# Performance work log

Measured on AMD Instinct MI355X. Metric: run time of the kernel, lower is better.

The kernel has to match this reference:

```python
import jax, jax.numpy as jnp
import numpy as np

B, N, C, K = 32, 4096, 768, 8

def setup_inputs() -> dict:
    key = jax.random.key(0)
    ks = jax.random.split(key, 5)
    x = jax.random.normal(ks[0], (B, N, C), dtype=jnp.float32)
    ln_gamma = jnp.ones((C,), dtype=jnp.float32)
    ln_beta = jnp.zeros((C,), dtype=jnp.float32)
    W1 = jax.random.normal(ks[1], (C, C), dtype=jnp.float32) / np.sqrt(C)
    b1 = jnp.zeros((C,), dtype=jnp.float32)
    W2 = jax.random.normal(ks[2], (C, K), dtype=jnp.float32) / np.sqrt(C)
    b2 = jnp.zeros((K,), dtype=jnp.float32)
    return {"x": x, "ln_gamma": ln_gamma, "ln_beta": ln_beta,
            "W1": W1, "b1": b1, "W2": W2, "b2": b2}

def reference(x, ln_gamma, ln_beta, W1, b1, W2, b2):
    # LayerNorm over last dim (eps matches torch default 1e-5)
    mu = jnp.mean(x, axis=-1, keepdims=True)
    var = jnp.mean(jnp.square(x - mu), axis=-1, keepdims=True)
    h = (x - mu) * jax.lax.rsqrt(var + 1e-5) * ln_gamma + ln_beta
    # Linear -> exact GELU -> Linear
    h = jax.nn.gelu(h @ W1 + b1, approximate=False)
    logits = h @ W2 + b2  # [B, N, K]
    # softmax over tokens (dim=1)
    attn = jax.nn.softmax(logits, axis=1)
    # weighted token pooling: [B,N,K],[B,N,C] -> [B,K,C]
    return jnp.einsum('bnk,bnc->bkc', attn, x)
```

## Files before the change

### kernel.cpp

```cpp
#include <hip/hip_runtime.h>
#include <hip/hip_fp16.h>

#define M_TOKENS (32*4096)
#define C_DIM 768
#define K_OUT 8

typedef _Float16 f16x8 __attribute__((ext_vector_type(8)));
typedef float f32x4 __attribute__((ext_vector_type(4)));

__device__ __forceinline__ void gl2lds16(const void* g, void* l) {
    __builtin_amdgcn_global_load_lds((const __attribute__((address_space(1))) void*)g,
                                     (__attribute__((address_space(3))) void*)l, 16, 0, 0);
}

__device__ __forceinline__ float gelu_exact(float x) {
    return 0.5f * x * (1.0f + erff(x * 0.70710678118654752440f));
}

__global__ __launch_bounds__(256) void prep_w1(const float* __restrict__ w1,
                                               const float* __restrict__ gamma,
                                               _Float16* __restrict__ w1t) {
    __shared__ float t[64][65];
    const int k0 = blockIdx.x * 64, n0 = blockIdx.y * 64;
    const int c = threadIdx.x & 63, r4 = threadIdx.x >> 6;
#pragma unroll
    for (int p = 0; p < 16; ++p) {
        const int r = p*4 + r4;
        t[r][c] = w1[(size_t)(k0 + r)*C_DIM + n0 + c];
    }
    __syncthreads();
    const float g = gamma[k0 + c];
#pragma unroll
    for (int p = 0; p < 16; ++p) {
        const int n = p*4 + r4;
        w1t[(size_t)(n0 + n)*C_DIM + k0 + c] = (_Float16)(t[c][n] * g);
    }
}

__global__ __launch_bounds__(256) void prep_b1(const float* __restrict__ w1,
                                               const float* __restrict__ beta,
                                               const float* __restrict__ b1,
                                               float* __restrict__ b1p) {
    __shared__ float red[256];
    const int nl = threadIdx.x & 63;
    const int n = blockIdx.x*64 + nl;
    const int part = threadIdx.x >> 6;
    float s = 0.f;
    for (int k = part*192; k < part*192 + 192; ++k)
        s += beta[k] * w1[(size_t)k*C_DIM + n];
    red[threadIdx.x] = s;
    __syncthreads();
    if (part == 0)
        b1p[n] = b1[n] + red[nl] + red[nl+64] + red[nl+128] + red[nl+192];
}


__global__ __launch_bounds__(256) void xnorm_kernel(const float* __restrict__ x,
                                                    _Float16* __restrict__ xn) {
    const int row = blockIdx.x*4 + (threadIdx.x >> 6);
    const int lane = threadIdx.x & 63;
    const float4* xr = (const float4*)(x + (size_t)row * C_DIM);
    float4 v[3];
    float s = 0.f, s2 = 0.f;
#pragma unroll
    for (int i = 0; i < 3; ++i) {
        v[i] = xr[lane + i*64];
        s  += v[i].x + v[i].y + v[i].z + v[i].w;
        s2 += v[i].x*v[i].x + v[i].y*v[i].y + v[i].z*v[i].z + v[i].w*v[i].w;
    }
#pragma unroll
    for (int m = 1; m < 64; m <<= 1) { s += __shfl_xor(s, m); s2 += __shfl_xor(s2, m); }
    const float mu = s * (1.f/768.f);
    const float rs = rsqrtf(s2 * (1.f/768.f) - mu*mu + 1e-5f);
    const float nm = -mu * rs;
    _Float16* xo = xn + (size_t)row * C_DIM;
#pragma unroll
    for (int i = 0; i < 3; ++i) {
        union { _Float16 h[4]; uint2 uu; } pk;
        pk.h[0] = (_Float16)(v[i].x*rs + nm);
        pk.h[1] = (_Float16)(v[i].y*rs + nm);
        pk.h[2] = (_Float16)(v[i].z*rs + nm);
        pk.h[3] = (_Float16)(v[i].w*rs + nm);
        *(uint2*)(xo + (size_t)(lane + i*64)*4) = pk.uu;
    }
}

__global__ __launch_bounds__(256) void gemm1_h_kernel(const _Float16* __restrict__ xn,
        const _Float16* __restrict__ w1t, const float* __restrict__ b1p,
        const float* __restrict__ w2, float* __restrict__ logits) {
    __shared__ __align__(16) union {
        struct { _Float16 a[128*64]; _Float16 b[128*64]; } s;
        _Float16 ht[128*136];
    } u;
    __shared__ float w2s[128*K_OUT];
    __shared__ float b1s[128];

    const int tid = threadIdx.x;
    const int wid = tid >> 6, lane = tid & 63;
    const int l15 = lane & 15, q = lane >> 4;
    const int wm = wid >> 1, wn = wid & 1;
    const int n0 = blockIdx.x * 128;
    const int m0 = blockIdx.y * 128;

    for (int i = tid; i < 128*K_OUT; i += 256) w2s[i] = w2[(size_t)n0*K_OUT + i];
    if (tid < 128) b1s[tid] = b1p[n0 + tid];

    f32x4 acc[4][4] = {};

    for (int kt = 0; kt < 12; ++kt) {
        const int k0 = kt * 64;
#pragma unroll
        for (int i = 0; i < 4; ++i) {
            const int L = i*256 + tid;
            const int row = L >> 3, j = (L & 7) ^ (row & 7);
            gl2lds16(xn + (size_t)(m0 + row)*C_DIM + k0 + j*8,
                     &u.s.a[(i*256 + wid*64)*8]);
        }
#pragma unroll
        for (int i = 0; i < 4; ++i) {
            const int L = i*256 + tid;
            const int row = L >> 3, j = (L & 7) ^ (row & 7);
            gl2lds16(w1t + (size_t)(n0 + row)*C_DIM + k0 + j*8,
                     &u.s.b[(i*256 + wid*64)*8]);
        }
        __syncthreads();
#pragma unroll
        for (int kk = 0; kk < 2; ++kk) {
            f16x8 af[4], bfr[4];
#pragma unroll
            for (int nt = 0; nt < 4; ++nt) {
                const int row = wn*64 + nt*16 + l15;
                const int j = (kk*4 + q) ^ (row & 7);
                af[nt] = *(const f16x8*)&u.s.b[row*64 + j*8];
            }
#pragma unroll
            for (int mt = 0; mt < 4; ++mt) {
                const int row = wm*64 + mt*16 + l15;
                const int j = (kk*4 + q) ^ (row & 7);
                bfr[mt] = *(const f16x8*)&u.s.a[row*64 + j*8];
            }
#pragma unroll
            for (int nt = 0; nt < 4; ++nt)
#pragma unroll
                for (int mt = 0; mt < 4; ++mt)
                    acc[nt][mt] = __builtin_amdgcn_mfma_f32_16x16x32_f16(
                        af[nt], bfr[mt], acc[nt][mt], 0, 0, 0);
        }
        __syncthreads();
    }

#pragma unroll
    for (int nt = 0; nt < 4; ++nt) {
#pragma unroll
        for (int mt = 0; mt < 4; ++mt) {
            const int token = wm*64 + mt*16 + l15;
            const int nl = wn*64 + nt*16 + q*4;
            union { _Float16 h[4]; uint2 uu; } pk;
#pragma unroll
            for (int r = 0; r < 4; ++r)
                pk.h[r] = (_Float16)gelu_exact(acc[nt][mt][r] + b1s[nl + r]);
            *(uint2*)&u.ht[token*136 + nl] = pk.uu;
        }
    }
    __syncthreads();

    f16x8 wf[4];
#pragma unroll
    for (int ks = 0; ks < 4; ++ks) {
        f16x8 t;
#pragma unroll
        for (int j = 0; j < 8; ++j) {
            const int kd = ks*32 + q*8 + j;
            t[j] = (_Float16)((l15 < K_OUT) ? w2s[kd*K_OUT + l15] : 0.f);
        }
        wf[ks] = t;
    }
#pragma unroll
    for (int t2 = 0; t2 < 2; ++t2) {
        const int tt = wid*2 + t2;
        f32x4 p = {};
#pragma unroll
        for (int ks = 0; ks < 4; ++ks) {
            const f16x8 a = *(const f16x8*)&u.ht[(tt*16 + l15)*136 + ks*32 + q*8];
            p = __builtin_amdgcn_mfma_f32_16x16x32_f16(a, wf[ks], p, 0, 0, 0);
        }
        if (l15 < K_OUT) {
#pragma unroll
            for (int r = 0; r < 4; ++r)
                atomicAdd(&logits[(size_t)(m0 + tt*16 + q*4 + r)*K_OUT + l15], p[r]);
        }
    }
}


__global__ __launch_bounds__(256) void stats_kernel(const float* __restrict__ x,
                                                    float2* __restrict__ stats) {
    const int row = blockIdx.x*4 + (threadIdx.x >> 6);
    const int lane = threadIdx.x & 63;
    const float4* xr = (const float4*)(x + (size_t)row * C_DIM);
    float s = 0.f, s2 = 0.f;
#pragma unroll
    for (int i = 0; i < 3; ++i) {
        const float4 v = xr[lane + i*64];
        s  += v.x + v.y + v.z + v.w;
        s2 += v.x*v.x + v.y*v.y + v.z*v.z + v.w*v.w;
    }
#pragma unroll
    for (int m = 1; m < 64; m <<= 1) { s += __shfl_xor(s, m); s2 += __shfl_xor(s2, m); }
    if (lane == 0) {
        const float mu = s * (1.f/768.f);
        const float rs = rsqrtf(s2 * (1.f/768.f) - mu*mu + 1e-5f);
        stats[row] = make_float2(rs, -mu*rs);
    }
}

__global__ __launch_bounds__(256) void gemm1_ln_kernel(const float* __restrict__ x,
        const float2* __restrict__ stats, const _Float16* __restrict__ w1t,
        const float* __restrict__ b1p, const float* __restrict__ w2,
        float* __restrict__ logits) {
    __shared__ __align__(16) union {
        struct { float a[128*64]; _Float16 b[128*64]; } s;
        _Float16 ht[128*136];
    } u;
    __shared__ float w2s[128*K_OUT];
    __shared__ float b1s[128];

    const int tid = threadIdx.x;
    const int wid = tid >> 6, lane = tid & 63;
    const int l15 = lane & 15, q = lane >> 4;
    const int wm = wid >> 1, wn = wid & 1;
    const int n0 = blockIdx.x * 128;
    const int m0 = blockIdx.y * 128;

    for (int i = tid; i < 128*K_OUT; i += 256) w2s[i] = w2[(size_t)n0*K_OUT + i];
    if (tid < 128) b1s[tid] = b1p[n0 + tid];

    float rsL[4], nmL[4];
#pragma unroll
    for (int mt = 0; mt < 4; ++mt) {
        const float2 st = stats[m0 + wm*64 + mt*16 + l15];
        rsL[mt] = st.x; nmL[mt] = st.y;
    }

    f32x4 acc[4][4] = {};

    for (int kt = 0; kt < 12; ++kt) {
        const int k0 = kt * 64;
#pragma unroll
        for (int i = 0; i < 8; ++i) {
            const int L = i*256 + tid;
            const int row = L >> 4, g = (L & 15) ^ (row & 15);
            gl2lds16(x + (size_t)(m0 + row)*C_DIM + k0 + g*4,
                     &u.s.a[(i*256 + wid*64)*4]);
        }
#pragma unroll
        for (int i = 0; i < 4; ++i) {
            const int L = i*256 + tid;
            const int row = L >> 3, j = (L & 7) ^ (row & 7);
            gl2lds16(w1t + (size_t)(n0 + row)*C_DIM + k0 + j*8,
                     &u.s.b[(i*256 + wid*64)*8]);
        }
        __syncthreads();
#pragma unroll
        for (int kk = 0; kk < 2; ++kk) {
            f16x8 af[4], bfr[4];
#pragma unroll
            for (int nt = 0; nt < 4; ++nt) {
                const int row = wn*64 + nt*16 + l15;
                const int j = (kk*4 + q) ^ (row & 7);
                af[nt] = *(const f16x8*)&u.s.b[row*64 + j*8];
            }
#pragma unroll
            for (int mt = 0; mt < 4; ++mt) {
                const int row = wm*64 + mt*16 + l15;
                const int gc = kk*8 + q*2;
                const int c0 = gc ^ (row & 15), c1 = (gc + 1) ^ (row & 15);
                const f32x4 v0 = *(const f32x4*)&u.s.a[row*64 + c0*4];
                const f32x4 v1 = *(const f32x4*)&u.s.a[row*64 + c1*4];
                f16x8 t;
#pragma unroll
                for (int j = 0; j < 4; ++j) {
                    t[j]   = (_Float16)(v0[j]*rsL[mt] + nmL[mt]);
                    t[4+j] = (_Float16)(v1[j]*rsL[mt] + nmL[mt]);
                }
                bfr[mt] = t;
            }
#pragma unroll
            for (int nt = 0; nt < 4; ++nt)
#pragma unroll
                for (int mt = 0; mt < 4; ++mt)
                    acc[nt][mt] = __builtin_amdgcn_mfma_f32_16x16x32_f16(
                        af[nt], bfr[mt], acc[nt][mt], 0, 0, 0);
        }
        __syncthreads();
    }

#pragma unroll
    for (int nt = 0; nt < 4; ++nt) {
#pragma unroll
        for (int mt = 0; mt < 4; ++mt) {
            const int token = wm*64 + mt*16 + l15;
            const int nl = wn*64 + nt*16 + q*4;
            union { _Float16 h[4]; uint2 uu; } pk;
#pragma unroll
            for (int r = 0; r < 4; ++r)
                pk.h[r] = (_Float16)gelu_exact(acc[nt][mt][r] + b1s[nl + r]);
            *(uint2*)&u.ht[token*136 + nl] = pk.uu;
        }
    }
    __syncthreads();

    f16x8 wf[4];
#pragma unroll
    for (int ks = 0; ks < 4; ++ks) {
        f16x8 t;
#pragma unroll
        for (int j = 0; j < 8; ++j) {
            const int kd = ks*32 + q*8 + j;
            t[j] = (_Float16)((l15 < K_OUT) ? w2s[kd*K_OUT + l15] : 0.f);
        }
        wf[ks] = t;
    }
#pragma unroll
    for (int t2 = 0; t2 < 2; ++t2) {
        const int tt = wid*2 + t2;
        f32x4 p = {};
#pragma unroll
        for (int ks = 0; ks < 4; ++ks) {
            const f16x8 a = *(const f16x8*)&u.ht[(tt*16 + l15)*136 + ks*32 + q*8];
            p = __builtin_amdgcn_mfma_f32_16x16x32_f16(a, wf[ks], p, 0, 0, 0);
        }
        if (l15 < K_OUT) {
#pragma unroll
            for (int r = 0; r < 4; ++r)
                atomicAdd(&logits[(size_t)(m0 + tt*16 + q*4 + r)*K_OUT + l15], p[r]);
        }
    }
}

__global__ __launch_bounds__(256) void softmax_kernel(float* p) {
    const int b = blockIdx.x >> 3, k = blockIdx.x & 7;
    const size_t base = ((size_t)b*4096)*K_OUT + k;
    const int tid = threadIdx.x;
    float r[16];
    float mx = -1e30f;
#pragma unroll
    for (int i = 0; i < 16; ++i) {
        r[i] = p[base + (size_t)(tid + i*256)*K_OUT];
        mx = fmaxf(mx, r[i]);
    }
#pragma unroll
    for (int m = 1; m < 64; m <<= 1) mx = fmaxf(mx, __shfl_xor(mx, m));
    __shared__ float redm[4], reds[4];
    if ((tid & 63) == 0) redm[tid >> 6] = mx;
    __syncthreads();
    mx = fmaxf(fmaxf(redm[0], redm[1]), fmaxf(redm[2], redm[3]));
    float s = 0.f;
#pragma unroll
    for (int i = 0; i < 16; ++i) { r[i] = __expf(r[i] - mx); s += r[i]; }
#pragma unroll
    for (int m = 1; m < 64; m <<= 1) s += __shfl_xor(s, m);
    if ((tid & 63) == 0) reds[tid >> 6] = s;
    __syncthreads();
    s = reds[0] + reds[1] + reds[2] + reds[3];
    const float inv = 1.f / s;
#pragma unroll
    for (int i = 0; i < 16; ++i)
        p[base + (size_t)(tid + i*256)*K_OUT] = r[i] * inv;
}

__global__ __launch_bounds__(192) void pool_kernel(const float* __restrict__ x,
        const float* __restrict__ attn, float* __restrict__ out) {
    const int b = blockIdx.x, nc = blockIdx.y;
    const int t0 = nc * 128;
    __shared__ float as_[128*K_OUT];
    for (int i = threadIdx.x; i < 128*K_OUT; i += 192)
        as_[i] = attn[((size_t)b*4096 + t0)*K_OUT + i];
    __syncthreads();
    const int c = threadIdx.x * 4;
    float acc[K_OUT][4] = {};
    const float* xb = x + ((size_t)b*4096 + t0)*C_DIM + c;
    for (int i = 0; i < 128; ++i) {
        const float4 xv = *(const float4*)(xb + (size_t)i*C_DIM);
#pragma unroll
        for (int k = 0; k < K_OUT; ++k) {
            const float a = as_[i*K_OUT + k];
            acc[k][0] += a*xv.x; acc[k][1] += a*xv.y;
            acc[k][2] += a*xv.z; acc[k][3] += a*xv.w;
        }
    }
#pragma unroll
    for (int k = 0; k < K_OUT; ++k)
#pragma unroll
        for (int j = 0; j < 4; ++j)
            atomicAdd(&out[((size_t)b*K_OUT + k)*C_DIM + c + j], acc[k][j]);
}

extern "C" void kernel_launch(void* const* d_in, const int* in_sizes, int n_in,
                              void* d_out, int out_size, void* d_ws, size_t ws_size,
                              hipStream_t stream) {
    const float* x     = (const float*)d_in[0];
    const float* gamma = (const float*)d_in[1];
    const float* beta  = (const float*)d_in[2];
    const float* W1    = (const float*)d_in[3];
    const float* b1    = (const float*)d_in[4];
    const float* W2    = (const float*)d_in[5];
    (void)in_sizes; (void)n_in;

    float* out = (float*)d_out;
    char* ws = (char*)d_ws;

    const size_t XN_BYTES  = (size_t)M_TOKENS * C_DIM * 2;
    const size_t NEED_NEW  = XN_BYTES + 1179648 + 4096 + 4194304;

    if (ws_size >= NEED_NEW) {
        _Float16* xn     = (_Float16*)ws;
        _Float16* w1t    = (_Float16*)(ws + XN_BYTES);
        float*    b1p    = (float*)(ws + XN_BYTES + 1179648);
        float*    logits = (float*)(ws + XN_BYTES + 1179648 + 4096);

        (void)hipMemsetAsync(logits, 0, (size_t)M_TOKENS * K_OUT * 4, stream);
        (void)hipMemsetAsync(d_out, 0, (size_t)out_size * sizeof(float), stream);

        prep_w1<<<dim3(12, 12), 256, 0, stream>>>(W1, gamma, w1t);
        prep_b1<<<12, 256, 0, stream>>>(W1, beta, b1, b1p);
        xnorm_kernel<<<M_TOKENS/4, 256, 0, stream>>>(x, xn);
        gemm1_h_kernel<<<dim3(6, 1024), 256, 0, stream>>>(xn, w1t, b1p, W2, logits);
        softmax_kernel<<<256, 256, 0, stream>>>(logits);
        pool_kernel<<<dim3(32, 32), 192, 0, stream>>>(x, logits, out);
    } else {
        float2*   stats  = (float2*)ws;
        _Float16* w1t    = (_Float16*)(ws + 1048576);
        float*    b1p    = (float*)(ws + 2228224);
        float*    logits = (float*)(ws + 2232320);

        (void)hipMemsetAsync(logits, 0, (size_t)M_TOKENS * K_OUT * 4, stream);
        (void)hipMemsetAsync(d_out, 0, (size_t)out_size * sizeof(float), stream);

        prep_w1<<<dim3(12, 12), 256, 0, stream>>>(W1, gamma, w1t);
        prep_b1<<<12, 256, 0, stream>>>(W1, beta, b1, b1p);
        stats_kernel<<<M_TOKENS/4, 256, 0, stream>>>(x, stats);
        gemm1_ln_kernel<<<dim3(6, 1024), 256, 0, stream>>>(x, stats, w1t, b1p, W2, logits);
        softmax_kernel<<<256, 256, 0, stream>>>(logits);
        pool_kernel<<<dim3(32, 32), 192, 0, stream>>>(x, logits, out);
    }
}
```

Measured before the change: 1.079 ms.

## Use polynomial erf GELU, two rows per xnorm wave, swizzled GEMM tiles, unroll pool

Result: faster. 1.006 ms (-6.8%).

```diff
diff --git a/kernel.cpp b/kernel.cpp
--- a/kernel.cpp
+++ b/kernel.cpp
@@ -13,8 +13,20 @@
                                      (__attribute__((address_space(3))) void*)l, 16, 0, 0);
 }
 
-__device__ __forceinline__ float gelu_exact(float x) {
-    return 0.5f * x * (1.0f + erff(x * 0.70710678118654752440f));
+__device__ __forceinline__ float gelu_fast(float x) {
+    const float z  = x * 0.70710678118654752440f;
+    const float az = fabsf(z);
+    const float t  = __builtin_amdgcn_rcpf(1.0f + 0.3275911f * az);
+    float p = 1.061405429f;
+    p = p * t - 1.453152027f;
+    p = p * t + 1.421413741f;
+    p = p * t - 0.284496736f;
+    p = p * t + 0.254829592f;
+    p = p * t;
+    const float e = __expf(-az * az);
+    const float erf_abs = 1.0f - p * e;
+    const float erf_z = copysignf(erf_abs, z);
+    return 0.5f * x * (1.0f + erf_z);
 }
 
 __global__ __launch_bounds__(256) void prep_w1(const float* __restrict__ w1,
@@ -54,34 +66,49 @@
         b1p[n] = b1[n] + red[nl] + red[nl+64] + red[nl+128] + red[nl+192];
 }
 
-
 __global__ __launch_bounds__(256) void xnorm_kernel(const float* __restrict__ x,
                                                     _Float16* __restrict__ xn) {
-    const int row = blockIdx.x*4 + (threadIdx.x >> 6);
+    const int row0 = blockIdx.x*8 + (threadIdx.x >> 6)*2;
     const int lane = threadIdx.x & 63;
-    const float4* xr = (const float4*)(x + (size_t)row * C_DIM);
-    float4 v[3];
-    float s = 0.f, s2 = 0.f;
+    const float4* xr0 = (const float4*)(x + (size_t)row0 * C_DIM);
+    const float4* xr1 = (const float4*)(x + (size_t)(row0 + 1) * C_DIM);
+    float4 v0[3], v1[3];
+#pragma unroll
+    for (int i = 0; i < 3; ++i) { v0[i] = xr0[lane + i*64]; v1[i] = xr1[lane + i*64]; }
+    float sa = 0.f, s2a = 0.f, sb = 0.f, s2b = 0.f;
 #pragma unroll
     for (int i = 0; i < 3; ++i) {
-        v[i] = xr[lane + i*64];
-        s  += v[i].x + v[i].y + v[i].z + v[i].w;
-        s2 += v[i].x*v[i].x + v[i].y*v[i].y + v[i].z*v[i].z + v[i].w*v[i].w;
-    }
-#pragma unroll
-    for (int m = 1; m < 64; m <<= 1) { s += __shfl_xor(s, m); s2 += __shfl_xor(s2, m); }
-    const float mu = s * (1.f/768.f);
-    const float rs = rsqrtf(s2 * (1.f/768.f) - mu*mu + 1e-5f);
-    const float nm = -mu * rs;
-    _Float16* xo = xn + (size_t)row * C_DIM;
+        sa  += v0[i].x + v0[i].y + v0[i].z + v0[i].w;
+        s2a += v0[i].x*v0[i].x + v0[i].y*v0[i].y + v0[i].z*v0[i].z + v0[i].w*v0[i].w;
+        sb  += v1[i].x + v1[i].y + v1[i].z + v1[i].w;
+        s2b += v1[i].x*v1[i].x + v1[i].y*v1[i].y + v1[i].z*v1[i].z + v1[i].w*v1[i].w;
+    }
+#pragma unroll
+    for (int m = 1; m < 64; m <<= 1) {
+        sa += __shfl_xor(sa, m); s2a += __shfl_xor(s2a, m);
+        sb += __shfl_xor(sb, m); s2b += __shfl_xor(s2b, m);
+    }
+    const float mua = sa * (1.f/768.f);
+    const float rsa = rsqrtf(s2a * (1.f/768.f) - mua*mua + 1e-5f);
+    const float nma = -mua * rsa;
+    const float mub = sb * (1.f/768.f);
+    const float rsb = rsqrtf(s2b * (1.f/768.f) - mub*mub + 1e-5f);
+    const float nmb = -mub * rsb;
+    _Float16* xo0 = xn + (size_t)row0 * C_DIM;
+    _Float16* xo1 = xn + (size_t)(row0 + 1) * C_DIM;
 #pragma unroll
     for (int i = 0; i < 3; ++i) {
         union { _Float16 h[4]; uint2 uu; } pk;
-        pk.h[0] = (_Float16)(v[i].x*rs + nm);
-        pk.h[1] = (_Float16)(v[i].y*rs + nm);
-        pk.h[2] = (_Float16)(v[i].z*rs + nm);
-        pk.h[3] = (_Float16)(v[i].w*rs + nm);
-        *(uint2*)(xo + (size_t)(lane + i*64)*4) = pk.uu;
+        pk.h[0] = (_Float16)(v0[i].x*rsa + nma);
+        pk.h[1] = (_Float16)(v0[i].y*rsa + nma);
+        pk.h[2] = (_Float16)(v0[i].z*rsa + nma);
+        pk.h[3] = (_Float16)(v0[i].w*rsa + nma);
+        *(uint2*)(xo0 + (size_t)(lane + i*64)*4) = pk.uu;
+        pk.h[0] = (_Float16)(v1[i].x*rsb + nmb);
+        pk.h[1] = (_Float16)(v1[i].y*rsb + nmb);
+        pk.h[2] = (_Float16)(v1[i].z*rsb + nmb);
+        pk.h[3] = (_Float16)(v1[i].w*rsb + nmb);
+        *(uint2*)(xo1 + (size_t)(lane + i*64)*4) = pk.uu;
     }
 }
 
@@ -99,8 +126,11 @@
     const int wid = tid >> 6, lane = tid & 63;
     const int l15 = lane & 15, q = lane >> 4;
     const int wm = wid >> 1, wn = wid & 1;
-    const int n0 = blockIdx.x * 128;
-    const int m0 = blockIdx.y * 128;
+
+    const int L = blockIdx.y * 6 + blockIdx.x;
+    const int swz = (L & 7) * 768 + (L >> 3);
+    const int n0 = (swz % 6) * 128;
+    const int m0 = (swz / 6) * 128;
 
     for (int i = tid; i < 128*K_OUT; i += 256) w2s[i] = w2[(size_t)n0*K_OUT + i];
     if (tid < 128) b1s[tid] = b1p[n0 + tid];
@@ -111,15 +141,15 @@
         const int k0 = kt * 64;
 #pragma unroll
         for (int i = 0; i < 4; ++i) {
-            const int L = i*256 + tid;
-            const int row = L >> 3, j = (L & 7) ^ (row & 7);
+            const int Li = i*256 + tid;
+            const int row = Li >> 3, j = (Li & 7) ^ (row & 7);
             gl2lds16(xn + (size_t)(m0 + row)*C_DIM + k0 + j*8,
                      &u.s.a[(i*256 + wid*64)*8]);
         }
 #pragma unroll
         for (int i = 0; i < 4; ++i) {
-            const int L = i*256 + tid;
-            const int row = L >> 3, j = (L & 7) ^ (row & 7);
+            const int Li = i*256 + tid;
+            const int row = Li >> 3, j = (Li & 7) ^ (row & 7);
             gl2lds16(w1t + (size_t)(n0 + row)*C_DIM + k0 + j*8,
                      &u.s.b[(i*256 + wid*64)*8]);
         }
@@ -158,7 +188,7 @@
             union { _Float16 h[4]; uint2 uu; } pk;
 #pragma unroll
             for (int r = 0; r < 4; ++r)
-                pk.h[r] = (_Float16)gelu_exact(acc[nt][mt][r] + b1s[nl + r]);
+                pk.h[r] = (_Float16)gelu_fast(acc[nt][mt][r] + b1s[nl + r]);
             *(uint2*)&u.ht[token*136 + nl] = pk.uu;
         }
     }
@@ -304,7 +334,7 @@
             union { _Float16 h[4]; uint2 uu; } pk;
 #pragma unroll
             for (int r = 0; r < 4; ++r)
-                pk.h[r] = (_Float16)gelu_exact(acc[nt][mt][r] + b1s[nl + r]);
+                pk.h[r] = (_Float16)gelu_fast(acc[nt][mt][r] + b1s[nl + r]);
             *(uint2*)&u.ht[token*136 + nl] = pk.uu;
         }
     }
@@ -380,6 +410,7 @@
     const int c = threadIdx.x * 4;
     float acc[K_OUT][4] = {};
     const float* xb = x + ((size_t)b*4096 + t0)*C_DIM + c;
+#pragma unroll 4
     for (int i = 0; i < 128; ++i) {
         const float4 xv = *(const float4*)(xb + (size_t)i*C_DIM);
 #pragma unroll
@@ -424,7 +455,7 @@
 
         prep_w1<<<dim3(12, 12), 256, 0, stream>>>(W1, gamma, w1t);
         prep_b1<<<12, 256, 0, stream>>>(W1, beta, b1, b1p);
-        xnorm_kernel<<<M_TOKENS/4, 256, 0, stream>>>(x, xn);
+        xnorm_kernel<<<M_TOKENS/8, 256, 0, stream>>>(x, xn);
         gemm1_h_kernel<<<dim3(6, 1024), 256, 0, stream>>>(xn, w1t, b1p, W2, logits);
         softmax_kernel<<<256, 256, 0, stream>>>(logits);
         pool_kernel<<<dim3(32, 32), 192, 0, stream>>>(x, logits, out);
```
